# Optimization experiments

Hardware: AMD Instinct MI355X
Metric: run time of the kernel (lower is better)

## Reference

```python
import jax, jax.numpy as jnp
import numpy as np
from jax import lax

N, M, B = 512, 1024, 1024  # signal dim, atoms, batch (batch==m required by X = W @ Gamma)
POWER_ITER = 100
IHT_ITER = 50


def setup_inputs() -> dict:
    key = jax.random.key(0)
    k1, k2 = jax.random.split(key)
    Y = jax.random.normal(k1, (B, N), dtype=jnp.float32)
    W = jax.random.normal(k2, (N, M), dtype=jnp.float32)
    return {"Y": Y, "W": W, "K": 64}


def power_method(W):
    # 100 iterations of X <- X W^T W / ||.||; returns last pre-normalization norm
    # (approx largest eigenvalue of W^T W), matching PowerMethod in the source.
    X0 = jax.random.normal(jax.random.key(42), (1, W.shape[1]), dtype=W.dtype)

    def body(i, carry):
        X, _ = carry
        X2 = (X @ W.T) @ W          # [1, m]
        nm = jnp.linalg.norm(X2)
        return (X2 / nm, nm)

    _, nm = lax.fori_loop(0, POWER_ITER, body, (X0, jnp.asarray(1.0, W.dtype)))
    return nm


def hard_threshold_k(G, K):
    # keep entries strictly larger (in abs) than the (K+1)-th largest per row
    a = jnp.sort(jnp.abs(G), axis=1)[:, ::-1]   # descending per row
    T = a[:, K][:, None]                          # [B, 1]
    return G * (jnp.abs(G) > T).astype(G.dtype)


def reference(Y, W, K):
    # NormDict: column-normalize the dictionary
    W = W / jnp.linalg.norm(W, axis=0)
    c = power_method(W)
    eta = 1.0 / c
    Yn = jnp.linalg.norm(Y)

    # IHT sparse coding
    Gamma = hard_threshold_k(Y @ (eta * W), K)     # [B, m]
    residual = Gamma @ W.T - Y                      # [B, n]

    def step(carry, _):
        Gamma, residual = carry
        Gamma = hard_threshold_k(Gamma - eta * (residual @ W), K)
        residual = Gamma @ W.T - Y
        return (Gamma, residual), jnp.linalg.norm(residual) / Yn

    (Gamma, residual), norms = lax.scan(step, (Gamma, residual), None, length=IHT_ITER)

    X = W @ Gamma  # [n, m] @ [B, m] -> requires B == m, as in the torch source
    return X, Gamma, norms
```

## Files before the change

kernel.cpp:

```cpp
#include <hip/hip_runtime.h>


#define DEV __device__ __forceinline__

constexpr int Nd = 512;
constexpr int Md = 1024;
constexpr int Bd = 1024;
constexpr int Ksp = 64;
constexpr int IHT = 50;

DEV float wave_reduce_f(float v) {
#pragma unroll
  for (int off = 32; off > 0; off >>= 1) v += __shfl_down(v, off);
  return v;
}
DEV double wave_reduce_d(double v) {
#pragma unroll
  for (int off = 32; off > 0; off >>= 1) v += __shfl_down(v, off);
  return v;
}
DEV float rfl_f(float v) {
  return __uint_as_float(__builtin_amdgcn_readfirstlane(__float_as_uint(v)));
}

__global__ void k_zero(double* dacc) {
  int t = threadIdx.x;
  if (t < 51) dacc[t] = 0.0;
}

__global__ __launch_bounds__(256) void k_colnorm(const float* __restrict__ W,
                                                 float* __restrict__ cnorm) {
  int col = blockIdx.x * 256 + threadIdx.x;
  double ss = 0.0;
  for (int i = 0; i < Nd; ++i) {
    float w = W[(size_t)i * Md + col];
    ss = fma((double)w, (double)w, ss);
  }
  cnorm[col] = (float)sqrt(ss);
}

__global__ __launch_bounds__(256) void k_normalize(const float* __restrict__ W,
                                                   const float* __restrict__ cnorm,
                                                   float* __restrict__ Wn) {
  int idx = blockIdx.x * 256 + threadIdx.x;
  Wn[idx] = W[idx] / cnorm[idx & (Md - 1)];
}

__global__ __launch_bounds__(256) void k_yn2(const float* __restrict__ Y,
                                             double* __restrict__ dacc) {
  double s = 0.0;
  for (int i = blockIdx.x * 256 + threadIdx.x; i < Bd * Nd; i += gridDim.x * 256) {
    float y = Y[i];
    s = fma((double)y, (double)y, s);
  }
  s = wave_reduce_d(s);
  __shared__ double red[4];
  int lane = threadIdx.x & 63, wid = threadIdx.x >> 6;
  if (lane == 0) red[wid] = s;
  __syncthreads();
  if (threadIdx.x == 0) atomicAdd(&dacc[0], red[0] + red[1] + red[2] + red[3]);
}

template <int BM, int BN, int TN>
__global__ __launch_bounds__(256) void k_gemm_t(const float* __restrict__ A, int lda, int ta,
                                                const float* __restrict__ B, int ldb, int tb,
                                                float* __restrict__ C, int ldc, int Kd,
                                                float scale) {
  constexpr int AE = 32 * BM / 256;
  constexpr int BE = 32 * BN / 256;
  __shared__ __align__(16) float As[32][BM + 4];
  __shared__ __align__(16) float Bs[32][BN + 4];
  const int tid = threadIdx.x;
  const int tx = tid % (BN / TN), ty = tid / (BN / TN);
  const int m0 = blockIdx.y * BM, n0 = blockIdx.x * BN;
  float ra[AE], rb[BE];
  float acc[4][TN];
#pragma unroll
  for (int i = 0; i < 4; ++i)
#pragma unroll
    for (int j = 0; j < TN; ++j) acc[i][j] = 0.f;

  auto loadA = [&](int k0) {
    if (!ta) {
      const int c = tid & 31, r0 = tid >> 5;
#pragma unroll
      for (int i = 0; i < AE; ++i)
        ra[i] = A[(size_t)(m0 + r0 + i * 8) * lda + (k0 + c)];
    } else {
      const int r = tid % BM, c0 = tid / BM;
#pragma unroll
      for (int i = 0; i < AE; ++i)
        ra[i] = A[(size_t)(k0 + c0 + i * (256 / BM)) * lda + (m0 + r)];
    }
  };
  auto storeA = [&]() {
    if (!ta) {
      const int c = tid & 31, r0 = tid >> 5;
#pragma unroll
      for (int i = 0; i < AE; ++i) As[c][r0 + i * 8] = ra[i];
    } else {
      const int r = tid % BM, c0 = tid / BM;
#pragma unroll
      for (int i = 0; i < AE; ++i) As[c0 + i * (256 / BM)][r] = ra[i];
    }
  };
  auto loadB = [&](int k0) {
    if (!tb) {
      const int c = tid % BN, r0 = tid / BN;
#pragma unroll
      for (int i = 0; i < BE; ++i)
        rb[i] = B[(size_t)(k0 + r0 + i * (256 / BN)) * ldb + (n0 + c)];
    } else {
      const int r = tid & 31, c0 = tid >> 5;
#pragma unroll
      for (int i = 0; i < BE; ++i)
        rb[i] = B[(size_t)(n0 + c0 + i * 8) * ldb + (k0 + r)];
    }
  };
  auto storeB = [&]() {
    if (!tb) {
      const int c = tid % BN, r0 = tid / BN;
#pragma unroll
      for (int i = 0; i < BE; ++i) Bs[r0 + i * (256 / BN)][c] = rb[i];
    } else {
      const int r = tid & 31, c0 = tid >> 5;
#pragma unroll
      for (int i = 0; i < BE; ++i) Bs[r][c0 + i * 8] = rb[i];
    }
  };

  loadA(0);
  loadB(0);
  storeA();
  storeB();
  __syncthreads();
  for (int k0 = 0; k0 < Kd; k0 += 32) {
    const bool more = (k0 + 32) < Kd;
    if (more) { loadA(k0 + 32); loadB(k0 + 32); }
#pragma unroll
    for (int kk = 0; kk < 32; ++kk) {
      const float4 a4 = *(const float4*)&As[kk][ty * 4];
      const float aa[4] = {a4.x, a4.y, a4.z, a4.w};
      float bb[TN];
      if constexpr (TN == 4) {
        const float4 b4 = *(const float4*)&Bs[kk][tx * 4];
        bb[0] = b4.x; bb[1] = b4.y; bb[2] = b4.z; bb[3] = b4.w;
      } else {
        const float2 b2 = *(const float2*)&Bs[kk][tx * 2];
        bb[0] = b2.x; bb[1] = b2.y;
      }
#pragma unroll
      for (int i = 0; i < 4; ++i)
#pragma unroll
        for (int j = 0; j < TN; ++j) acc[i][j] = fmaf(aa[i], bb[j], acc[i][j]);
    }
    if (more) {
      __syncthreads();
      storeA();
      storeB();
      __syncthreads();
    }
  }
#pragma unroll
  for (int i = 0; i < 4; ++i) {
    if constexpr (TN == 4) {
      float4 o;
      o.x = acc[i][0] * scale; o.y = acc[i][1] * scale;
      o.z = acc[i][2] * scale; o.w = acc[i][3] * scale;
      *(float4*)&C[(size_t)(m0 + ty * 4 + i) * ldc + n0 + tx * 4] = o;
    } else {
      float2 o;
      o.x = acc[i][0] * scale; o.y = acc[i][1] * scale;
      *(float2*)&C[(size_t)(m0 + ty * 4 + i) * ldc + n0 + tx * 2] = o;
    }
  }
}

DEV float erfinv_xla(float x) {
  float w = -log1pf(-x * x);
  float p;
  if (w < 5.0f) {
    w = w - 2.5f;
    p = 2.81022636e-08f;
    p = fmaf(p, w, 3.43273939e-07f);
    p = fmaf(p, w, -3.5233877e-06f);
    p = fmaf(p, w, -4.39150654e-06f);
    p = fmaf(p, w, 0.00021858087f);
    p = fmaf(p, w, -0.00125372503f);
    p = fmaf(p, w, -0.00417768164f);
    p = fmaf(p, w, 0.246640727f);
    p = fmaf(p, w, 1.50140941f);
  } else {
    w = sqrtf(w) - 3.0f;
    p = -0.000200214257f;
    p = fmaf(p, w, 0.000100950558f);
    p = fmaf(p, w, 0.00134934322f);
    p = fmaf(p, w, -0.00367342844f);
    p = fmaf(p, w, 0.00573950773f);
    p = fmaf(p, w, -0.0076224613f);
    p = fmaf(p, w, 0.00943887047f);
    p = fmaf(p, w, 1.00167406f);
    p = fmaf(p, w, 2.83297682f);
  }
  return p * x;
}

#define TF_ROUND(r)                                  \
  {                                                  \
    x0 += x1;                                        \
    x1 = (x1 << (r)) | (x1 >> (32 - (r)));           \
    x1 ^= x0;                                        \
  }

__global__ void k_x0(float* __restrict__ X0) {
  unsigned i = threadIdx.x;
  unsigned x0 = i, x1 = i + 512u;
  const unsigned ks0 = 0u, ks1 = 42u, ks2 = 0x1BD11BDAu ^ 42u;
  x0 += ks0; x1 += ks1;
  TF_ROUND(13) TF_ROUND(15) TF_ROUND(26) TF_ROUND(6)  x0 += ks1; x1 += ks2 + 1u;
  TF_ROUND(17) TF_ROUND(29) TF_ROUND(16) TF_ROUND(24) x0 += ks2; x1 += ks0 + 2u;
  TF_ROUND(13) TF_ROUND(15) TF_ROUND(26) TF_ROUND(6)  x0 += ks0; x1 += ks1 + 3u;
  TF_ROUND(17) TF_ROUND(29) TF_ROUND(16) TF_ROUND(24) x0 += ks1; x1 += ks2 + 4u;
  TF_ROUND(13) TF_ROUND(15) TF_ROUND(26) TF_ROUND(6)  x0 += ks2; x1 += ks0 + 5u;
  const float lo = -0.99999994f;
  const float sqrt2 = 1.41421356237f;
  {
    float f = __uint_as_float((x0 >> 9) | 0x3f800000u) - 1.0f;
    float u = fmaxf(lo, f * 2.0f + lo);
    X0[i] = sqrt2 * erfinv_xla(u);
  }
  {
    float f = __uint_as_float((x1 >> 9) | 0x3f800000u) - 1.0f;
    float u = fmaxf(lo, f * 2.0f + lo);
    X0[i + 512] = sqrt2 * erfinv_xla(u);
  }
}

__global__ __launch_bounds__(256) void k_z0(const float* __restrict__ X0,
                                            const float* __restrict__ Wn,
                                            float* __restrict__ vout) {
  const int lane = threadIdx.x & 63, wid = threadIdx.x >> 6;
  const int row = blockIdx.x * 4 + wid;
  const float4* wr = (const float4*)(Wn + (size_t)row * Md);
  const float4* x4 = (const float4*)X0;
  float s = 0.f;
#pragma unroll
  for (int e = 0; e < 4; ++e) {
    const float4 w4 = wr[lane + e * 64];
    const float4 xx = x4[lane + e * 64];
    s = fmaf(w4.x, xx.x, s); s = fmaf(w4.y, xx.y, s);
    s = fmaf(w4.z, xx.z, s); s = fmaf(w4.w, xx.w, s);
  }
  s = wave_reduce_f(s);
  if (lane == 0) vout[row] = s;
}

__global__ __launch_bounds__(256) void k_pmv(const float* __restrict__ Mmat,
                                             const float* __restrict__ vin,
                                             float* __restrict__ vout, float scale) {
  const int lane = threadIdx.x & 63, wid = threadIdx.x >> 6;
  const int row = blockIdx.x * 4 + wid;
  const float4* mr = (const float4*)(Mmat + (size_t)row * Nd);
  const float4* v4 = (const float4*)vin;
  float s = 0.f;
#pragma unroll
  for (int e = 0; e < 2; ++e) {
    const float4 m4 = mr[lane + e * 64];
    const float4 xx = v4[lane + e * 64];
    s = fmaf(m4.x, xx.x, s); s = fmaf(m4.y, xx.y, s);
    s = fmaf(m4.z, xx.z, s); s = fmaf(m4.w, xx.w, s);
  }
  s = wave_reduce_f(s);
  if (lane == 0) vout[row] = s * scale;
}

__global__ __launch_bounds__(512) void k_pfinal(const float* __restrict__ v99,
                                                const float* __restrict__ v100,
                                                float* __restrict__ cbuf) {
  __shared__ double r99[8], r100[8];
  const int t = threadIdx.x, lane = t & 63, wid = t >> 6;
  double a = (double)v99[t]; a *= a;
  double b = (double)v100[t]; b *= b;
  a = wave_reduce_d(a);
  b = wave_reduce_d(b);
  if (lane == 0) { r99[wid] = a; r100[wid] = b; }
  __syncthreads();
  if (t == 0) {
    double n99 = 0.0, n100 = 0.0;
    for (int i = 0; i < 8; ++i) { n99 += r99[i]; n100 += r100[i]; }
    float c = (float)(8.0 * sqrt(n100 / n99));
    cbuf[0] = c;
    cbuf[1] = 1.0f / c;
  }
}

__global__ __launch_bounds__(256) void k_iht_all(
    const float* __restrict__ Q, const float* __restrict__ YW,
    const float* __restrict__ cbuf, float* __restrict__ gdense,
    double* __restrict__ normacc) {
  __shared__ float u[Md];
  __shared__ float yws[Md];
  __shared__ float sval[Ksp];
  __shared__ int sidx[Ksp];
  __shared__ unsigned histbuf[2][4][256];
  __shared__ unsigned wred[4];
  __shared__ unsigned sel_need, sel_prefix;
  __shared__ double dred[4];
  __shared__ int scnt;

  const int t = threadIdx.x;
  const int b = blockIdx.x;
  const int lane = t & 63, wv = t >> 6;
  const float eta = cbuf[1];
  const float4 yw = ((const float4*)(YW + (size_t)b * Md))[t];
  ((float4*)yws)[t] = yw;
#pragma unroll
  for (int e = 0; e < 8; ++e) ((unsigned*)histbuf)[t + e * 256] = 0u;
  const float* Qt = Q + t * 4;

  for (int it = -1; it < IHT; ++it) {
    if (it >= 0) {
      const int cnt = scnt;
      float4 p = make_float4(0.f, 0.f, 0.f, 0.f);
      int k = 0;
      for (; k + 8 <= cnt; k += 8) {
#define GROW(j)                                                        \
        const int id##j = __builtin_amdgcn_readfirstlane(sidx[k + j]); \
        const float g##j = rfl_f(sval[k + j]);                         \
        const float4 q##j = *(const float4*)(Qt + (size_t)id##j * Md);
        GROW(0) GROW(1) GROW(2) GROW(3) GROW(4) GROW(5) GROW(6) GROW(7)
#undef GROW
        p.x = fmaf(g0, q0.x, p.x); p.x = fmaf(g1, q1.x, p.x);
        p.x = fmaf(g2, q2.x, p.x); p.x = fmaf(g3, q3.x, p.x);
        p.x = fmaf(g4, q4.x, p.x); p.x = fmaf(g5, q5.x, p.x);
        p.x = fmaf(g6, q6.x, p.x); p.x = fmaf(g7, q7.x, p.x);
        p.y = fmaf(g0, q0.y, p.y); p.y = fmaf(g1, q1.y, p.y);
        p.y = fmaf(g2, q2.y, p.y); p.y = fmaf(g3, q3.y, p.y);
        p.y = fmaf(g4, q4.y, p.y); p.y = fmaf(g5, q5.y, p.y);
        p.y = fmaf(g6, q6.y, p.y); p.y = fmaf(g7, q7.y, p.y);
        p.z = fmaf(g0, q0.z, p.z); p.z = fmaf(g1, q1.z, p.z);
        p.z = fmaf(g2, q2.z, p.z); p.z = fmaf(g3, q3.z, p.z);
        p.z = fmaf(g4, q4.z, p.z); p.z = fmaf(g5, q5.z, p.z);
        p.z = fmaf(g6, q6.z, p.z); p.z = fmaf(g7, q7.z, p.z);
        p.w = fmaf(g0, q0.w, p.w); p.w = fmaf(g1, q1.w, p.w);
        p.w = fmaf(g2, q2.w, p.w); p.w = fmaf(g3, q3.w, p.w);
        p.w = fmaf(g4, q4.w, p.w); p.w = fmaf(g5, q5.w, p.w);
        p.w = fmaf(g6, q6.w, p.w); p.w = fmaf(g7, q7.w, p.w);
      }
      for (; k < cnt; ++k) {
        const int id = __builtin_amdgcn_readfirstlane(sidx[k]);
        const float g = rfl_f(sval[k]);
        const float4 q = *(const float4*)(Qt + (size_t)id * Md);
        p.x = fmaf(g, q.x, p.x); p.y = fmaf(g, q.y, p.y);
        p.z = fmaf(g, q.z, p.z); p.w = fmaf(g, q.w, p.w);
      }
      ((float4*)u)[t] = p;
      __syncthreads();
      if (it >= 1) {
        double part = 0.0;
        if (t < cnt) {
          const int id = sidx[t];
          part = (double)sval[t] * ((double)u[id] - 2.0 * (double)yws[id]);
        }
        part = wave_reduce_d(part);
        if (lane == 0) dred[wv] = part;
      }
      __syncthreads();
      if (it >= 1 && t == 0)
        atomicAdd(&normacc[it - 1], dred[0] + dred[1] + dred[2] + dred[3]);
      float4 uu;
      uu.x = -(eta * (p.x - yw.x)); uu.y = -(eta * (p.y - yw.y));
      uu.z = -(eta * (p.z - yw.z)); uu.w = -(eta * (p.w - yw.w));
      ((float4*)u)[t] = uu;
      __syncthreads();
      if (t < cnt) u[sidx[t]] += sval[t];
      __syncthreads();
    } else {
      float4 uu;
      uu.x = eta * yw.x; uu.y = eta * yw.y; uu.z = eta * yw.z; uu.w = eta * yw.w;
      ((float4*)u)[t] = uu;
      __syncthreads();
    }

    float vals[4];
    unsigned key[4];
    {
      const float4 mv = ((const float4*)u)[t];
      vals[0] = mv.x; vals[1] = mv.y; vals[2] = mv.z; vals[3] = mv.w;
#pragma unroll
      for (int e = 0; e < 4; ++e) key[e] = __float_as_uint(vals[e]) & 0x7fffffffu;
    }

    unsigned need = Ksp + 1, prefix = 0u, pmask = 0u;
#pragma unroll
    for (int pass = 3; pass >= 0; --pass) {
      const int sh = 8 * pass;
      const int pb = pass & 1;
      unsigned(*hist)[256] = histbuf[pb];
#pragma unroll
      for (int e = 0; e < 4; ++e)
        if ((key[e] & pmask) == prefix) atomicAdd(&hist[wv][(key[e] >> sh) & 255u], 1u);
      __syncthreads();
      unsigned* hz = histbuf[pb ^ 1][wv];
      hz[lane] = 0u; hz[lane + 64] = 0u; hz[lane + 128] = 0u; hz[lane + 192] = 0u;
      if (wv == 0) {
        const unsigned c0 = hist[0][lane] + hist[1][lane] + hist[2][lane] + hist[3][lane];
        const unsigned c1 = hist[0][lane + 64] + hist[1][lane + 64] + hist[2][lane + 64] + hist[3][lane + 64];
        const unsigned c2 = hist[0][lane + 128] + hist[1][lane + 128] + hist[2][lane + 128] + hist[3][lane + 128];
        const unsigned c3 = hist[0][lane + 192] + hist[1][lane + 192] + hist[2][lane + 192] + hist[3][lane + 192];
        unsigned s0 = c0, s1 = c1, s2 = c2, s3 = c3;
#pragma unroll
        for (int off = 1; off < 64; off <<= 1) {
          const unsigned y0 = __shfl_down(s0, off), y1 = __shfl_down(s1, off);
          const unsigned y2 = __shfl_down(s2, off), y3 = __shfl_down(s3, off);
          if (lane + off < 64) { s0 += y0; s1 += y1; s2 += y2; s3 += y3; }
        }
        const unsigned T1 = __builtin_amdgcn_readfirstlane(s1);
        const unsigned T2 = __builtin_amdgcn_readfirstlane(s2);
        const unsigned T3 = __builtin_amdgcn_readfirstlane(s3);
        const unsigned i0 = s0 + T1 + T2 + T3;
        const unsigned i1 = s1 + T2 + T3;
        const unsigned i2 = s2 + T3;
        const unsigned i3 = s3;
        if (i0 >= need && i0 - c0 < need) { sel_prefix = prefix | ((unsigned)lane << sh); sel_need = need - (i0 - c0); }
        if (i1 >= need && i1 - c1 < need) { sel_prefix = prefix | ((unsigned)(lane + 64) << sh); sel_need = need - (i1 - c1); }
        if (i2 >= need && i2 - c2 < need) { sel_prefix = prefix | ((unsigned)(lane + 128) << sh); sel_need = need - (i2 - c2); }
        if (i3 >= need && i3 - c3 < need) { sel_prefix = prefix | ((unsigned)(lane + 192) << sh); sel_need = need - (i3 - c3); }
      }
      __syncthreads();
      prefix = sel_prefix;
      need = sel_need;
      pmask |= (255u << sh);
    }
    const unsigned Tbits = prefix;

    unsigned keep = 0u;
    unsigned myc = 0u;
#pragma unroll
    for (int e = 0; e < 4; ++e)
      if (key[e] > Tbits) { keep |= (1u << e); ++myc; }
    unsigned x = myc;
#pragma unroll
    for (int off = 1; off < 64; off <<= 1) {
      const unsigned y = __shfl_up(x, off);
      if (lane >= off) x += y;
    }
    if (lane == 63) wred[wv] = x;
    __syncthreads();
    unsigned addlo = 0u;
    for (int w2 = 0; w2 < wv; ++w2) addlo += wred[w2];
    int base = (int)(x + addlo) - (int)myc;
#pragma unroll
    for (int e = 0; e < 4; ++e) {
      if (keep & (1u << e)) {
        sidx[base] = t * 4 + e;
        sval[base] = vals[e];
        ++base;
      }
    }
    if (t == 0) scnt = (int)(wred[0] + wred[1] + wred[2] + wred[3]);
    if (it == IHT - 1) {
      float4 g;
      g.x = (keep & 1u) ? vals[0] : 0.f;
      g.y = (keep & 2u) ? vals[1] : 0.f;
      g.z = (keep & 4u) ? vals[2] : 0.f;
      g.w = (keep & 8u) ? vals[3] : 0.f;
      ((float4*)(gdense + (size_t)b * Md))[t] = g;
    }
    __syncthreads();
  }

  const int cnt = scnt;
  if (wv == 0) {
    double part = 0.0;
    if (lane < cnt) {
      const int id = sidx[lane];
      float acc2 = 0.f;
      for (int k = 0; k < cnt; ++k)
        acc2 = fmaf(sval[k], Q[(size_t)sidx[k] * Md + id], acc2);
      part = (double)sval[lane] * ((double)acc2 - 2.0 * (double)yws[id]);
    }
    part = wave_reduce_d(part);
    if (lane == 0) atomicAdd(&normacc[IHT - 1], part);
  }
}

__global__ void k_wnorms(const double* __restrict__ dacc, float* __restrict__ onorms) {
  const int t = threadIdx.x;
  if (t < IHT) {
    const double yn2 = dacc[0];
    double r2 = yn2 + dacc[1 + t];
    if (r2 < 0.0) r2 = 0.0;
    onorms[t] = (float)(sqrt(r2) / sqrt(yn2));
  }
}

extern "C" void kernel_launch(void* const* d_in, const int* in_sizes, int n_in,
                              void* d_out, int out_size, void* d_ws, size_t ws_size,
                              hipStream_t stream) {
  (void)in_sizes; (void)n_in; (void)out_size; (void)ws_size;
  const float* Y = (const float*)d_in[0];
  const float* W = (const float*)d_in[1];
  float* out = (float*)d_out;
  float* outX = out;
  float* outG = out + Nd * Md;
  float* outN = outG + Bd * Md;

  char* wsb = (char*)d_ws;
  double* dacc = (double*)wsb;
  float* cbuf = (float*)(wsb + 512);
  float* Wn = (float*)(wsb + 1024);
  float* Q = Wn + Nd * Md;
  float* YW = Q + Md * Md;
  float* Smat = YW + Bd * Md;
  float* S2 = Smat + Nd * Nd;
  float* cnorm = S2 + Nd * Nd;
  float* X0 = cnorm + Md;
  float* V = X0 + Md;

  k_zero<<<1, 64, 0, stream>>>(dacc);
  k_colnorm<<<4, 256, 0, stream>>>(W, cnorm);
  k_normalize<<<2048, 256, 0, stream>>>(W, cnorm, Wn);

  k_gemm_t<64, 32, 2><<<dim3(16, 8), 256, 0, stream>>>(Wn, Md, 0, Wn, Md, 1, Smat, Nd, Md, 1.0f);
  k_gemm_t<64, 32, 2><<<dim3(16, 8), 256, 0, stream>>>(Smat, Nd, 0, Smat, Nd, 0, S2, Nd, Nd, 0.015625f);
  k_gemm_t<64, 64, 4><<<dim3(16, 16), 256, 0, stream>>>(Wn, Md, 1, Wn, Md, 0, Q, Md, Nd, 1.0f);
  k_gemm_t<64, 64, 4><<<dim3(16, 16), 256, 0, stream>>>(Y, Nd, 0, Wn, Md, 0, YW, Md, Nd, 1.0f);
  k_yn2<<<128, 256, 0, stream>>>(Y, dacc);

  k_x0<<<1, 512, 0, stream>>>(X0);
  k_z0<<<128, 256, 0, stream>>>(X0, Wn, V);
  float* pin = V;
  float* pout = V + 512;
  for (int i = 0; i < 49; ++i) {
    k_pmv<<<128, 256, 0, stream>>>(S2, pin, pout, 1.0f);
    float* tp = pin; pin = pout; pout = tp;
  }
  k_pmv<<<128, 256, 0, stream>>>(Smat, pin, V + 1024, 0.125f);
  k_pmv<<<128, 256, 0, stream>>>(Smat, V + 1024, V + 1536, 0.125f);
  k_pfinal<<<1, 512, 0, stream>>>(V + 1024, V + 1536, cbuf);

  k_iht_all<<<1024, 256, 0, stream>>>(Q, YW, cbuf, outG, dacc + 1);
  k_wnorms<<<1, 64, 0, stream>>>(dacc, outN);

  k_gemm_t<64, 32, 2><<<dim3(32, 8), 256, 0, stream>>>(Wn, Md, 0, outG, Md, 0, outX, Md, Md, 1.0f);
}
```

Measured before the change: 983.2 us.

## Restructure IHT loop to cut barriers, pipeline Q gathers, fuse small launches

After: 938.4 us. 4.5% less time.

```diff
diff --git a/kernel.cpp b/kernel.cpp
--- a/kernel.cpp
+++ b/kernel.cpp
@@ -23,13 +23,10 @@
   return __uint_as_float(__builtin_amdgcn_readfirstlane(__float_as_uint(v)));
 }
 
-__global__ void k_zero(double* dacc) {
-  int t = threadIdx.x;
-  if (t < 51) dacc[t] = 0.0;
-}
-
 __global__ __launch_bounds__(256) void k_colnorm(const float* __restrict__ W,
-                                                 float* __restrict__ cnorm) {
+                                                 float* __restrict__ cnorm,
+                                                 double* __restrict__ dacc) {
+  if (blockIdx.x == 0 && threadIdx.x < 51) dacc[threadIdx.x] = 0.0;
   int col = blockIdx.x * 256 + threadIdx.x;
   double ss = 0.0;
   for (int i = 0; i < Nd; ++i) {
@@ -212,8 +209,7 @@
     x1 ^= x0;                                        \
   }
 
-__global__ void k_x0(float* __restrict__ X0) {
-  unsigned i = threadIdx.x;
+DEV float x0_value(unsigned i, int hi) {
   unsigned x0 = i, x1 = i + 512u;
   const unsigned ks0 = 0u, ks1 = 42u, ks2 = 0x1BD11BDAu ^ 42u;
   x0 += ks0; x1 += ks1;
@@ -224,25 +220,25 @@
   TF_ROUND(13) TF_ROUND(15) TF_ROUND(26) TF_ROUND(6)  x0 += ks2; x1 += ks0 + 5u;
   const float lo = -0.99999994f;
   const float sqrt2 = 1.41421356237f;
-  {
-    float f = __uint_as_float((x0 >> 9) | 0x3f800000u) - 1.0f;
-    float u = fmaxf(lo, f * 2.0f + lo);
-    X0[i] = sqrt2 * erfinv_xla(u);
-  }
-  {
-    float f = __uint_as_float((x1 >> 9) | 0x3f800000u) - 1.0f;
-    float u = fmaxf(lo, f * 2.0f + lo);
-    X0[i + 512] = sqrt2 * erfinv_xla(u);
-  }
-}
-
-__global__ __launch_bounds__(256) void k_z0(const float* __restrict__ X0,
-                                            const float* __restrict__ Wn,
+  const unsigned bits = hi ? x1 : x0;
+  float f = __uint_as_float((bits >> 9) | 0x3f800000u) - 1.0f;
+  float u = fmaxf(lo, f * 2.0f + lo);
+  return sqrt2 * erfinv_xla(u);
+}
+
+__global__ __launch_bounds__(256) void k_z0(const float* __restrict__ Wn,
                                             float* __restrict__ vout) {
-  const int lane = threadIdx.x & 63, wid = threadIdx.x >> 6;
+  __shared__ float x0s[Md];
+  const int t = threadIdx.x;
+  x0s[t] = x0_value((unsigned)t, 0);
+  x0s[t + 512] = x0_value((unsigned)t, 1);
+  x0s[t + 256] = x0_value((unsigned)(t + 256), 0);
+  x0s[t + 768] = x0_value((unsigned)(t + 256), 1);
+  __syncthreads();
+  const int lane = t & 63, wid = t >> 6;
   const int row = blockIdx.x * 4 + wid;
   const float4* wr = (const float4*)(Wn + (size_t)row * Md);
-  const float4* x4 = (const float4*)X0;
+  const float4* x4 = (const float4*)x0s;
   float s = 0.f;
 #pragma unroll
   for (int e = 0; e < 4; ++e) {
@@ -294,7 +290,7 @@
   }
 }
 
-__global__ __launch_bounds__(256) void k_iht_all(
+__global__ __launch_bounds__(256, 4) void k_iht_all(
     const float* __restrict__ Q, const float* __restrict__ YW,
     const float* __restrict__ cbuf, float* __restrict__ gdense,
     double* __restrict__ normacc) {
@@ -305,7 +301,7 @@
   __shared__ unsigned histbuf[2][4][256];
   __shared__ unsigned wred[4];
   __shared__ unsigned sel_need, sel_prefix;
-  __shared__ double dred[4];
+  __shared__ double dred0;
   __shared__ int scnt;
 
   const int t = threadIdx.x;
@@ -317,35 +313,79 @@
 #pragma unroll
   for (int e = 0; e < 8; ++e) ((unsigned*)histbuf)[t + e * 256] = 0u;
   const float* Qt = Q + t * 4;
+  float gdr[4] = {0.f, 0.f, 0.f, 0.f};
+
+  auto scan_select = [&](unsigned(*hist)[256], unsigned pfx, unsigned nd, int sh) {
+    const unsigned c0 = hist[0][lane] + hist[1][lane] + hist[2][lane] + hist[3][lane];
+    const unsigned c1 = hist[0][lane + 64] + hist[1][lane + 64] + hist[2][lane + 64] + hist[3][lane + 64];
+    const unsigned c2 = hist[0][lane + 128] + hist[1][lane + 128] + hist[2][lane + 128] + hist[3][lane + 128];
+    const unsigned c3 = hist[0][lane + 192] + hist[1][lane + 192] + hist[2][lane + 192] + hist[3][lane + 192];
+    unsigned s0 = c0, s1 = c1, s2 = c2, s3 = c3;
+#pragma unroll
+    for (int off = 1; off < 64; off <<= 1) {
+      const unsigned y0 = __shfl_down(s0, off), y1 = __shfl_down(s1, off);
+      const unsigned y2 = __shfl_down(s2, off), y3 = __shfl_down(s3, off);
+      if (lane + off < 64) { s0 += y0; s1 += y1; s2 += y2; s3 += y3; }
+    }
+    const unsigned T1 = __builtin_amdgcn_readfirstlane(s1);
+    const unsigned T2 = __builtin_amdgcn_readfirstlane(s2);
+    const unsigned T3 = __builtin_amdgcn_readfirstlane(s3);
+    const unsigned i0 = s0 + T1 + T2 + T3;
+    const unsigned i1 = s1 + T2 + T3;
+    const unsigned i2 = s2 + T3;
+    const unsigned i3 = s3;
+    if (i0 >= nd && i0 - c0 < nd) { sel_prefix = pfx | ((unsigned)lane << sh); sel_need = nd - (i0 - c0); }
+    if (i1 >= nd && i1 - c1 < nd) { sel_prefix = pfx | ((unsigned)(lane + 64) << sh); sel_need = nd - (i1 - c1); }
+    if (i2 >= nd && i2 - c2 < nd) { sel_prefix = pfx | ((unsigned)(lane + 128) << sh); sel_need = nd - (i2 - c2); }
+    if (i3 >= nd && i3 - c3 < nd) { sel_prefix = pfx | ((unsigned)(lane + 192) << sh); sel_need = nd - (i3 - c3); }
+  };
 
   for (int it = -1; it < IHT; ++it) {
+    float vals[4];
+    unsigned key[4];
+    int cnt = 0;
     if (it >= 0) {
-      const int cnt = scnt;
+      cnt = scnt;
       float4 p = make_float4(0.f, 0.f, 0.f, 0.f);
+      float4 qa[8], qb[8];
+      float ga[8], gb[8];
+      auto LOAD8 = [&](float4* q, float* g, int kk) {
+#pragma unroll
+        for (int j = 0; j < 8; ++j) {
+          const int id = __builtin_amdgcn_readfirstlane(sidx[kk + j]);
+          g[j] = rfl_f(sval[kk + j]);
+          q[j] = *(const float4*)(Qt + (size_t)id * Md);
+        }
+      };
+      auto FMA8 = [&](const float4* q, const float* g) {
+#pragma unroll
+        for (int j = 0; j < 8; ++j) p.x = fmaf(g[j], q[j].x, p.x);
+#pragma unroll
+        for (int j = 0; j < 8; ++j) p.y = fmaf(g[j], q[j].y, p.y);
+#pragma unroll
+        for (int j = 0; j < 8; ++j) p.z = fmaf(g[j], q[j].z, p.z);
+#pragma unroll
+        for (int j = 0; j < 8; ++j) p.w = fmaf(g[j], q[j].w, p.w);
+      };
       int k = 0;
-      for (; k + 8 <= cnt; k += 8) {
-#define GROW(j)                                                        \
-        const int id##j = __builtin_amdgcn_readfirstlane(sidx[k + j]); \
-        const float g##j = rfl_f(sval[k + j]);                         \
-        const float4 q##j = *(const float4*)(Qt + (size_t)id##j * Md);
-        GROW(0) GROW(1) GROW(2) GROW(3) GROW(4) GROW(5) GROW(6) GROW(7)
-#undef GROW
-        p.x = fmaf(g0, q0.x, p.x); p.x = fmaf(g1, q1.x, p.x);
-        p.x = fmaf(g2, q2.x, p.x); p.x = fmaf(g3, q3.x, p.x);
-        p.x = fmaf(g4, q4.x, p.x); p.x = fmaf(g5, q5.x, p.x);
-        p.x = fmaf(g6, q6.x, p.x); p.x = fmaf(g7, q7.x, p.x);
-        p.y = fmaf(g0, q0.y, p.y); p.y = fmaf(g1, q1.y, p.y);
-        p.y = fmaf(g2, q2.y, p.y); p.y = fmaf(g3, q3.y, p.y);
-        p.y = fmaf(g4, q4.y, p.y); p.y = fmaf(g5, q5.y, p.y);
-        p.y = fmaf(g6, q6.y, p.y); p.y = fmaf(g7, q7.y, p.y);
-        p.z = fmaf(g0, q0.z, p.z); p.z = fmaf(g1, q1.z, p.z);
-        p.z = fmaf(g2, q2.z, p.z); p.z = fmaf(g3, q3.z, p.z);
-        p.z = fmaf(g4, q4.z, p.z); p.z = fmaf(g5, q5.z, p.z);
-        p.z = fmaf(g6, q6.z, p.z); p.z = fmaf(g7, q7.z, p.z);
-        p.w = fmaf(g0, q0.w, p.w); p.w = fmaf(g1, q1.w, p.w);
-        p.w = fmaf(g2, q2.w, p.w); p.w = fmaf(g3, q3.w, p.w);
-        p.w = fmaf(g4, q4.w, p.w); p.w = fmaf(g5, q5.w, p.w);
-        p.w = fmaf(g6, q6.w, p.w); p.w = fmaf(g7, q7.w, p.w);
+      const int nfull = cnt & ~7;
+      if (nfull >= 8) {
+        LOAD8(qa, ga, 0);
+        k = 8;
+        for (; k + 16 <= nfull; k += 16) {
+          LOAD8(qb, gb, k);
+          FMA8(qa, ga);
+          LOAD8(qa, ga, k + 8);
+          FMA8(qb, gb);
+        }
+        if (k + 8 <= nfull) {
+          LOAD8(qb, gb, k);
+          FMA8(qa, ga);
+          FMA8(qb, gb);
+          k += 8;
+        } else {
+          FMA8(qa, ga);
+        }
       }
       for (; k < cnt; ++k) {
         const int id = __builtin_amdgcn_readfirstlane(sidx[k]);
@@ -355,78 +395,56 @@
         p.z = fmaf(g, q.z, p.z); p.w = fmaf(g, q.w, p.w);
       }
       ((float4*)u)[t] = p;
+      vals[0] = -(eta * (p.x - yw.x)) + gdr[0];
+      vals[1] = -(eta * (p.y - yw.y)) + gdr[1];
+      vals[2] = -(eta * (p.z - yw.z)) + gdr[2];
+      vals[3] = -(eta * (p.w - yw.w)) + gdr[3];
+    } else {
+      vals[0] = eta * yw.x; vals[1] = eta * yw.y;
+      vals[2] = eta * yw.z; vals[3] = eta * yw.w;
       __syncthreads();
+    }
+#pragma unroll
+    for (int e = 0; e < 4; ++e) key[e] = __float_as_uint(vals[e]) & 0x7fffffffu;
+
+#pragma unroll
+    for (int e = 0; e < 4; ++e) atomicAdd(&histbuf[1][wv][key[e] >> 24], 1u);
+    __syncthreads();
+    if (wv == 0) {
+      scan_select(histbuf[1], 0u, Ksp + 1, 24);
+    } else if (wv == 1) {
       if (it >= 1) {
         double part = 0.0;
-        if (t < cnt) {
-          const int id = sidx[t];
-          part = (double)sval[t] * ((double)u[id] - 2.0 * (double)yws[id]);
+        if (lane < cnt) {
+          const int id = sidx[lane];
+          part = (double)sval[lane] * ((double)u[id] - 2.0 * (double)yws[id]);
         }
         part = wave_reduce_d(part);
-        if (lane == 0) dred[wv] = part;
+        if (lane == 0) dred0 = part;
       }
-      __syncthreads();
-      if (it >= 1 && t == 0)
-        atomicAdd(&normacc[it - 1], dred[0] + dred[1] + dred[2] + dred[3]);
-      float4 uu;
-      uu.x = -(eta * (p.x - yw.x)); uu.y = -(eta * (p.y - yw.y));
-      uu.z = -(eta * (p.z - yw.z)); uu.w = -(eta * (p.w - yw.w));
-      ((float4*)u)[t] = uu;
-      __syncthreads();
-      if (t < cnt) u[sidx[t]] += sval[t];
-      __syncthreads();
-    } else {
-      float4 uu;
-      uu.x = eta * yw.x; uu.y = eta * yw.y; uu.z = eta * yw.z; uu.w = eta * yw.w;
-      ((float4*)u)[t] = uu;
-      __syncthreads();
-    }
-
-    float vals[4];
-    unsigned key[4];
-    {
-      const float4 mv = ((const float4*)u)[t];
-      vals[0] = mv.x; vals[1] = mv.y; vals[2] = mv.z; vals[3] = mv.w;
-#pragma unroll
-      for (int e = 0; e < 4; ++e) key[e] = __float_as_uint(vals[e]) & 0x7fffffffu;
-    }
-
-    unsigned need = Ksp + 1, prefix = 0u, pmask = 0u;
-#pragma unroll
-    for (int pass = 3; pass >= 0; --pass) {
+    } else {
+      unsigned* hz = (unsigned*)histbuf[0] + (wv - 2) * 512;
+#pragma unroll
+      for (int e = 0; e < 8; ++e) hz[lane + e * 64] = 0u;
+    }
+    __syncthreads();
+    unsigned prefix = sel_prefix;
+    unsigned need = sel_need;
+    unsigned pmask = 0xFF000000u;
+
+#pragma unroll
+    for (int pass = 2; pass >= 0; --pass) {
       const int sh = 8 * pass;
       const int pb = pass & 1;
       unsigned(*hist)[256] = histbuf[pb];
 #pragma unroll
       for (int e = 0; e < 4; ++e)
         if ((key[e] & pmask) == prefix) atomicAdd(&hist[wv][(key[e] >> sh) & 255u], 1u);
+      if (pass == 2 && it >= 1 && t == 0) atomicAdd(&normacc[it - 1], dred0);
       __syncthreads();
       unsigned* hz = histbuf[pb ^ 1][wv];
       hz[lane] = 0u; hz[lane + 64] = 0u; hz[lane + 128] = 0u; hz[lane + 192] = 0u;
-      if (wv == 0) {
-        const unsigned c0 = hist[0][lane] + hist[1][lane] + hist[2][lane] + hist[3][lane];
-        const unsigned c1 = hist[0][lane + 64] + hist[1][lane + 64] + hist[2][lane + 64] + hist[3][lane + 64];
-        const unsigned c2 = hist[0][lane + 128] + hist[1][lane + 128] + hist[2][lane + 128] + hist[3][lane + 128];
-        const unsigned c3 = hist[0][lane + 192] + hist[1][lane + 192] + hist[2][lane + 192] + hist[3][lane + 192];
-        unsigned s0 = c0, s1 = c1, s2 = c2, s3 = c3;
-#pragma unroll
-        for (int off = 1; off < 64; off <<= 1) {
-          const unsigned y0 = __shfl_down(s0, off), y1 = __shfl_down(s1, off);
-          const unsigned y2 = __shfl_down(s2, off), y3 = __shfl_down(s3, off);
-          if (lane + off < 64) { s0 += y0; s1 += y1; s2 += y2; s3 += y3; }
-        }
-        const unsigned T1 = __builtin_amdgcn_readfirstlane(s1);
-        const unsigned T2 = __builtin_amdgcn_readfirstlane(s2);
-        const unsigned T3 = __builtin_amdgcn_readfirstlane(s3);
-        const unsigned i0 = s0 + T1 + T2 + T3;
-        const unsigned i1 = s1 + T2 + T3;
-        const unsigned i2 = s2 + T3;
-        const unsigned i3 = s3;
-        if (i0 >= need && i0 - c0 < need) { sel_prefix = prefix | ((unsigned)lane << sh); sel_need = need - (i0 - c0); }
-        if (i1 >= need && i1 - c1 < need) { sel_prefix = prefix | ((unsigned)(lane + 64) << sh); sel_need = need - (i1 - c1); }
-        if (i2 >= need && i2 - c2 < need) { sel_prefix = prefix | ((unsigned)(lane + 128) << sh); sel_need = need - (i2 - c2); }
-        if (i3 >= need && i3 - c3 < need) { sel_prefix = prefix | ((unsigned)(lane + 192) << sh); sel_need = need - (i3 - c3); }
-      }
+      if (wv == 0) scan_select(hist, prefix, need, sh);
       __syncthreads();
       prefix = sel_prefix;
       need = sel_need;
@@ -439,6 +457,10 @@
 #pragma unroll
     for (int e = 0; e < 4; ++e)
       if (key[e] > Tbits) { keep |= (1u << e); ++myc; }
+    gdr[0] = (keep & 1u) ? vals[0] : 0.f;
+    gdr[1] = (keep & 2u) ? vals[1] : 0.f;
+    gdr[2] = (keep & 4u) ? vals[2] : 0.f;
+    gdr[3] = (keep & 8u) ? vals[3] : 0.f;
     unsigned x = myc;
 #pragma unroll
     for (int off = 1; off < 64; off <<= 1) {
@@ -461,10 +483,7 @@
     if (t == 0) scnt = (int)(wred[0] + wred[1] + wred[2] + wred[3]);
     if (it == IHT - 1) {
       float4 g;
-      g.x = (keep & 1u) ? vals[0] : 0.f;
-      g.y = (keep & 2u) ? vals[1] : 0.f;
-      g.z = (keep & 4u) ? vals[2] : 0.f;
-      g.w = (keep & 8u) ? vals[3] : 0.f;
+      g.x = gdr[0]; g.y = gdr[1]; g.z = gdr[2]; g.w = gdr[3];
       ((float4*)(gdense + (size_t)b * Md))[t] = g;
     }
     __syncthreads();
@@ -518,8 +537,7 @@
   float* X0 = cnorm + Md;
   float* V = X0 + Md;
 
-  k_zero<<<1, 64, 0, stream>>>(dacc);
-  k_colnorm<<<4, 256, 0, stream>>>(W, cnorm);
+  k_colnorm<<<4, 256, 0, stream>>>(W, cnorm, dacc);
   k_normalize<<<2048, 256, 0, stream>>>(W, cnorm, Wn);
 
   k_gemm_t<64, 32, 2><<<dim3(16, 8), 256, 0, stream>>>(Wn, Md, 0, Wn, Md, 1, Smat, Nd, Md, 1.0f);
@@ -528,8 +546,7 @@
   k_gemm_t<64, 64, 4><<<dim3(16, 16), 256, 0, stream>>>(Y, Nd, 0, Wn, Md, 0, YW, Md, Nd, 1.0f);
   k_yn2<<<128, 256, 0, stream>>>(Y, dacc);
 
-  k_x0<<<1, 512, 0, stream>>>(X0);
-  k_z0<<<128, 256, 0, stream>>>(X0, Wn, V);
+  k_z0<<<128, 256, 0, stream>>>(Wn, V);
   float* pin = V;
   float* pout = V + 512;
   for (int i = 0; i < 49; ++i) {
```
